# Kernel optimization log

Measured on AMD Instinct MI355X. Metric: run time of the kernel, lower is better.

The kernel has to match this reference:

```python
import jax, jax.numpy as jnp
import numpy as np

PAD = 1
STRIDE = 1


def setup_inputs() -> dict:
    key = jax.random.key(0)
    k1, k2 = jax.random.split(key)
    B, C, H, W = 16, 64, 112, 112
    KS, O = 3, 128
    x = jax.random.normal(k1, (B, C, H, W), dtype=jnp.float32)
    # weight layout matches torch module: (in_channel, k, k, out_channel)
    weight = jax.random.normal(k2, (C, KS, KS, O), dtype=jnp.float32)
    return {"x": x, "weight": weight}


def reference(x, weight):
    # Original: pad -> im2col (B,Ho,Wo,C*k*k) -> matmul with weight.reshape(-1,O)
    # -> permute to (B,O,Ho,Wo). This is exactly a standard conv2d; we express
    # it as the fused implicit-GEMM convolution (same math, no huge intermediate).
    # Note: the module's _bias parameter is never used in forward, so no bias here.
    w_oihw = jnp.transpose(weight, (3, 0, 1, 2))  # (O, C, kh, kw)
    out = jax.lax.conv_general_dilated(
        x,
        w_oihw,
        window_strides=(STRIDE, STRIDE),
        padding=[(PAD, PAD), (PAD, PAD)],
        dimension_numbers=("NCHW", "OIHW", "NCHW"),
    )
    return out  # (B, O, Ho, Wo)
```

## Files before the change

kernel.cpp:

```cpp
#include <hip/hip_runtime.h>
#include <hip/hip_bf16.h>
#include <stdint.h>

typedef __attribute__((ext_vector_type(8))) short short8;
typedef __attribute__((ext_vector_type(4))) float f32x4;

#define B_   16
#define C_   64
#define H_   112
#define W_   112
#define O_   128
#define HP   114
#define HWP  (HP*HP)
#define HW   (H_*W_)
#define XPAD_BYTES ((size_t)B_*HWP*C_*2)
#define WBUF_BYTES (9*64*128*2)

__device__ __forceinline__ unsigned short f2bf(float f) {
    union { float f; uint32_t u; } v; v.f = f;
    uint32_t u = v.u;
    u += 0x7fffu + ((u >> 16) & 1u);
    return (unsigned short)(u >> 16);
}

__global__ void pad_transpose(const float* __restrict__ x,
                              unsigned short* __restrict__ xpad)
{
    __shared__ float tile[64][113];
    const int bh = blockIdx.x;
    const int b = bh / H_, h = bh % H_;
    const int t = threadIdx.x;

    const float* xr = x + ((size_t)b * C_ * HW) + (size_t)h * W_;
    #pragma unroll
    for (int i = 0; i < 28; ++i) {
        int flat = i * 256 + t;
        int c = flat / W_, w = flat % W_;
        tile[c][w] = xr[(size_t)c * HW + w];
    }
    __syncthreads();

    unsigned short* dst = xpad + ((size_t)(b * HP + h + 1) * HP + 1) * C_;
    #pragma unroll
    for (int j = 0; j < 7; ++j) {
        int flat = j * 256 + t;
        int w = flat >> 4, c = (flat & 15) * 4;
        ushort4 v;
        v.x = f2bf(tile[c + 0][w]);
        v.y = f2bf(tile[c + 1][w]);
        v.z = f2bf(tile[c + 2][w]);
        v.w = f2bf(tile[c + 3][w]);
        *(ushort4*)(dst + (size_t)w * C_ + c) = v;
    }
}

__global__ void wtrans(const float* __restrict__ wt, char* __restrict__ wbuf)
{
    int idx = blockIdx.x * 256 + threadIdx.x;
    int slice = idx >> 13;
    int rem = idx & 8191;
    int o = rem >> 6, c = rem & 63;
    int kh = slice / 3, kw = slice % 3;
    float f = wt[(((size_t)c * 3 + kh) * 3 + kw) * O_ + o];
    size_t dstb = (size_t)slice * 16384 + (size_t)o * 128
                + (size_t)(((c >> 3) ^ (o & 7)) << 4) + ((c & 7) << 1);
    *(unsigned short*)(wbuf + dstb) = f2bf(f);
}

__global__ __launch_bounds__(256, 2) void conv_gemm(
    const char* __restrict__ xpad,
    const char* __restrict__ wbuf,
    float* __restrict__ out)
{
    __shared__ char lds[32768];
    char* ldsA = lds;
    char* ldsB = lds + 16384;

    const int t = threadIdx.x;
    const int lane = t & 63, wid = t >> 6;
    const int wr = wid >> 1, wc = wid & 1;
    const int bid = blockIdx.x;
    const int b = bid / 98;
    const int ml0 = (bid % 98) * 128;

    const char* srcA[4];
    #pragma unroll
    for (int i = 0; i < 4; ++i) {
        int r = wid * 32 + i * 8 + (lane >> 3);
        int ml = ml0 + r;
        int h = ml / W_, w = ml - h * W_;
        srcA[i] = xpad + ((size_t)b * HWP + (size_t)h * HP + w) * 128
                + (((lane & 7) ^ (r & 7)) << 4);
    }

    f32x4 acc[4][4] = {};

    #pragma unroll
    for (int s = 0; s < 9; ++s) {
        const int kh = s / 3, kw = s % 3;
        const int shiftA = (kh * HP + kw) * 128;

        __syncthreads();
        #pragma unroll
        for (int i = 0; i < 4; ++i) {
            __builtin_amdgcn_global_load_lds(
                (const __attribute__((address_space(1))) void*)(srcA[i] + shiftA),
                (__attribute__((address_space(3))) void*)(ldsA + (wid * 32 + i * 8) * 128),
                16, 0, 0);
        }
        const char* wsl = wbuf + s * 16384 + wid * 4096 + lane * 16;
        #pragma unroll
        for (int i = 0; i < 4; ++i) {
            __builtin_amdgcn_global_load_lds(
                (const __attribute__((address_space(1))) void*)(wsl + i * 1024),
                (__attribute__((address_space(3))) void*)(ldsB + wid * 4096 + i * 1024),
                16, 0, 0);
        }
        __syncthreads();

        #pragma unroll
        for (int ks = 0; ks < 2; ++ks) {
            short8 av[4], bv[4];
            const int xr = ((ks * 4 + (lane >> 4)) ^ (lane & 7)) << 4;
            #pragma unroll
            for (int mf = 0; mf < 4; ++mf)
                av[mf] = *(const short8*)(ldsA + (wr * 64 + mf * 16 + (lane & 15)) * 128 + xr);
            #pragma unroll
            for (int nf = 0; nf < 4; ++nf)
                bv[nf] = *(const short8*)(ldsB + (wc * 64 + nf * 16 + (lane & 15)) * 128 + xr);
            #pragma unroll
            for (int mf = 0; mf < 4; ++mf)
                #pragma unroll
                for (int nf = 0; nf < 4; ++nf)
                    acc[mf][nf] = __builtin_amdgcn_mfma_f32_16x16x32_bf16(
                        av[mf], bv[nf], acc[mf][nf], 0, 0, 0);
        }
    }

    const int oc = wc * 64 + (lane & 15);
    const int mrow = ml0 + wr * 64 + ((lane >> 4) << 2);
    #pragma unroll
    for (int mf = 0; mf < 4; ++mf) {
        #pragma unroll
        for (int nf = 0; nf < 4; ++nf) {
            float* dst = out + ((size_t)(b * O_ + oc + nf * 16) * HW) + mrow + mf * 16;
            *(f32x4*)dst = acc[mf][nf];
        }
    }
}

extern "C" void kernel_launch(void* const* d_in, const int* in_sizes, int n_in,
                              void* d_out, int out_size, void* d_ws, size_t ws_size,
                              hipStream_t stream) {
    const float* x  = (const float*)d_in[0];
    const float* wt = (const float*)d_in[1];
    float* out = (float*)d_out;
    char* xpad = (char*)d_ws;
    char* wbuf = (char*)d_ws + XPAD_BYTES;

    hipMemsetAsync(xpad, 0, XPAD_BYTES, stream);
    hipLaunchKernelGGL(pad_transpose, dim3(B_ * H_), dim3(256), 0, stream,
                       x, (unsigned short*)xpad);
    hipLaunchKernelGGL(wtrans, dim3(288), dim3(256), 0, stream, wt, wbuf);
    hipLaunchKernelGGL(conv_gemm, dim3(1568), dim3(256), 0, stream,
                       xpad, wbuf, out);
}
```

Before: 78.74 us.

## Load input halo tile once into LDS, read weights directly from global

The conv kernel now loads one 384-row padded-input window into LDS up front and reuses it for all nine filter taps, instead of reloading an A tile per tap with barriers. Weights are pre-permuted into MFMA fragment order and read straight from global/cache into registers, which removes the B LDS buffer and the per-tap syncs. The full-buffer memset is replaced by zeroing only the border rows and columns inside pad_transpose, and block IDs are remapped for locality. This trades higher register pressure and a bigger up-front LDS load for far fewer barriers and less redundant global traffic.

```diff
diff --git a/kernel.cpp b/kernel.cpp
--- a/kernel.cpp
+++ b/kernel.cpp
@@ -14,7 +14,7 @@
 #define HWP  (HP*HP)
 #define HW   (H_*W_)
 #define XPAD_BYTES ((size_t)B_*HWP*C_*2)
-#define WBUF_BYTES (9*64*128*2)
+#define NROWS 384
 
 __device__ __forceinline__ unsigned short f2bf(float f) {
     union { float f; uint32_t u; } v; v.f = f;
@@ -38,6 +38,19 @@
         int c = flat / W_, w = flat % W_;
         tile[c][w] = xr[(size_t)c * HW + w];
     }
+
+    if (t < 64) {
+        size_t base = ((size_t)(b * HP + h + 1) * HP) * 64;
+        xpad[base + t] = 0;
+        xpad[base + (size_t)113 * 64 + t] = 0;
+    }
+    if (h == 0 || h == 111) {
+        const int row = (h == 0) ? 0 : 113;
+        size_t base = ((size_t)(b * HP + row) * HP) * 64;
+        ushort4 z4; z4.x = z4.y = z4.z = z4.w = 0;
+        for (int k = t; k < (HP * 64) / 4; k += 256)
+            *(ushort4*)(xpad + base + (size_t)k * 4) = z4;
+    }
     __syncthreads();
 
     unsigned short* dst = xpad + ((size_t)(b * HP + h + 1) * HP + 1) * C_;
@@ -54,17 +67,19 @@
     }
 }
 
-__global__ void wtrans(const float* __restrict__ wt, char* __restrict__ wbuf)
+__global__ void wtrans(const float* __restrict__ wt, unsigned short* __restrict__ wbuf)
 {
-    int idx = blockIdx.x * 256 + threadIdx.x;
-    int slice = idx >> 13;
-    int rem = idx & 8191;
-    int o = rem >> 6, c = rem & 63;
-    int kh = slice / 3, kw = slice % 3;
-    float f = wt[(((size_t)c * 3 + kh) * 3 + kw) * O_ + o];
-    size_t dstb = (size_t)slice * 16384 + (size_t)o * 128
-                + (size_t)(((c >> 3) ^ (o & 7)) << 4) + ((c & 7) << 1);
-    *(unsigned short*)(wbuf + dstb) = f2bf(f);
+    int f = blockIdx.x * 256 + threadIdx.x;
+    int j    = f & 7;
+    int lane = (f >> 3) & 63;
+    int nf   = (f >> 9) & 3;
+    int wc   = (f >> 11) & 1;
+    int ks   = (f >> 12) & 1;
+    int s    = f >> 13;
+    int o = wc * 64 + nf * 16 + (lane & 15);
+    int c = (ks * 4 + (lane >> 4)) * 8 + j;
+    int kh = s / 3, kw = s % 3;
+    wbuf[f] = f2bf(wt[(((size_t)c * 3 + kh) * 3 + kw) * O_ + o]);
 }
 
 __global__ __launch_bounds__(256, 2) void conv_gemm(
@@ -72,68 +87,71 @@
     const char* __restrict__ wbuf,
     float* __restrict__ out)
 {
-    __shared__ char lds[32768];
-    char* ldsA = lds;
-    char* ldsB = lds + 16384;
+    __shared__ char ldsA[NROWS * 128];
 
     const int t = threadIdx.x;
     const int lane = t & 63, wid = t >> 6;
     const int wr = wid >> 1, wc = wid & 1;
-    const int bid = blockIdx.x;
+    const int bid0 = blockIdx.x;
+    const int bid = (bid0 & 7) * 196 + (bid0 >> 3);
     const int b = bid / 98;
     const int ml0 = (bid % 98) * 128;
+    const int oh0 = ml0 / W_;
+    const int pbase = ml0 + 2 * oh0;
 
-    const char* srcA[4];
+    const char* plane = xpad + (size_t)b * ((size_t)HWP * 128);
     #pragma unroll
-    for (int i = 0; i < 4; ++i) {
-        int r = wid * 32 + i * 8 + (lane >> 3);
-        int ml = ml0 + r;
-        int h = ml / W_, w = ml - h * W_;
-        srcA[i] = xpad + ((size_t)b * HWP + (size_t)h * HP + w) * 128
-                + (((lane & 7) ^ (r & 7)) << 4);
+    for (int i = 0; i < 12; ++i) {
+        const int gbase = i * 256 + wid * 64;
+        const int g = gbase + lane;
+        const int r = g >> 3, ck = g & 7;
+        __builtin_amdgcn_global_load_lds(
+            (const __attribute__((address_space(1))) void*)
+                (plane + (size_t)(pbase + r) * 128 + ((ck ^ (r & 7)) << 4)),
+            (__attribute__((address_space(3))) void*)(ldsA + gbase * 16),
+            16, 0, 0);
     }
+    __syncthreads();
+
+    int rowb[4];
+    #pragma unroll
+    for (int mf = 0; mf < 4; ++mf) {
+        int ml = ml0 + wr * 64 + mf * 16 + (lane & 15);
+        int oh = ml / W_;
+        rowb[mf] = ml + 2 * oh - pbase;
+    }
+    const int kq = lane >> 4;
 
     f32x4 acc[4][4] = {};
 
     #pragma unroll
     for (int s = 0; s < 9; ++s) {
         const int kh = s / 3, kw = s % 3;
-        const int shiftA = (kh * HP + kw) * 128;
+        const int soff = kh * HP + kw;
 
-        __syncthreads();
+        short8 bv[2][4];
+        const char* wb = (const char*)wbuf + s * 16384 + wc * 4096 + lane * 16;
         #pragma unroll
-        for (int i = 0; i < 4; ++i) {
-            __builtin_amdgcn_global_load_lds(
-                (const __attribute__((address_space(1))) void*)(srcA[i] + shiftA),
-                (__attribute__((address_space(3))) void*)(ldsA + (wid * 32 + i * 8) * 128),
-                16, 0, 0);
-        }
-        const char* wsl = wbuf + s * 16384 + wid * 4096 + lane * 16;
-        #pragma unroll
-        for (int i = 0; i < 4; ++i) {
-            __builtin_amdgcn_global_load_lds(
-                (const __attribute__((address_space(1))) void*)(wsl + i * 1024),
-                (__attribute__((address_space(3))) void*)(ldsB + wid * 4096 + i * 1024),
-                16, 0, 0);
-        }
-        __syncthreads();
+        for (int ks = 0; ks < 2; ++ks)
+            #pragma unroll
+            for (int nf = 0; nf < 4; ++nf)
+                bv[ks][nf] = *(const short8*)(wb + ks * 8192 + nf * 1024);
 
         #pragma unroll
         for (int ks = 0; ks < 2; ++ks) {
-            short8 av[4], bv[4];
-            const int xr = ((ks * 4 + (lane >> 4)) ^ (lane & 7)) << 4;
+            short8 av[4];
             #pragma unroll
-            for (int mf = 0; mf < 4; ++mf)
-                av[mf] = *(const short8*)(ldsA + (wr * 64 + mf * 16 + (lane & 15)) * 128 + xr);
-            #pragma unroll
-            for (int nf = 0; nf < 4; ++nf)
-                bv[nf] = *(const short8*)(ldsB + (wc * 64 + nf * 16 + (lane & 15)) * 128 + xr);
+            for (int mf = 0; mf < 4; ++mf) {
+                const int lrow = rowb[mf] + soff;
+                const int ck = (ks * 4 + kq) ^ (lrow & 7);
+                av[mf] = *(const short8*)(ldsA + lrow * 128 + (ck << 4));
+            }
             #pragma unroll
             for (int mf = 0; mf < 4; ++mf)
                 #pragma unroll
                 for (int nf = 0; nf < 4; ++nf)
                     acc[mf][nf] = __builtin_amdgcn_mfma_f32_16x16x32_bf16(
-                        av[mf], bv[nf], acc[mf][nf], 0, 0, 0);
+                        av[mf], bv[ks][nf], acc[mf][nf], 0, 0, 0);
         }
     }
 
@@ -158,10 +176,10 @@
     char* xpad = (char*)d_ws;
     char* wbuf = (char*)d_ws + XPAD_BYTES;
 
-    hipMemsetAsync(xpad, 0, XPAD_BYTES, stream);
     hipLaunchKernelGGL(pad_transpose, dim3(B_ * H_), dim3(256), 0, stream,
                        x, (unsigned short*)xpad);
-    hipLaunchKernelGGL(wtrans, dim3(288), dim3(256), 0, stream, wt, wbuf);
+    hipLaunchKernelGGL(wtrans, dim3(288), dim3(256), 0, stream,
+                       wt, (unsigned short*)wbuf);
     hipLaunchKernelGGL(conv_gemm, dim3(1568), dim3(256), 0, stream,
                        xpad, wbuf, out);
 }
```

Result: faster. 64.11 us (-18.6%).
